# Optimization experiments

Hardware: AMD Instinct MI355X
Metric: run time of the kernel (lower is better)

## Reference

```python
import jax, jax.numpy as jnp
import numpy as np

B, VGEN, VINP, S, VOUT = 2048, 50000, 32000, 200, 50304


def setup_inputs() -> dict:
    key = jax.random.key(0)
    ks = jax.random.split(key, 7)
    gen_scores = jax.random.normal(ks[0], (B, VGEN), dtype=jnp.float32)   # unnormalized gen scores
    scores = jax.random.normal(ks[1], (B, S), dtype=jnp.float32)          # attention scores over input
    interp = jax.random.uniform(ks[2], (B, 1), dtype=jnp.float32)         # P(generate) vs P(copy)
    gen_zero_mask = jnp.ones((VGEN,), dtype=jnp.float32)                  # gen_zero mask (all-ones here)
    gen_to_out = jax.random.randint(ks[4], (VGEN,), 0, VOUT)              # gen vocab -> out vocab map
    inp_to_out = jax.random.randint(ks[5], (VINP,), 0, VOUT)              # inp vocab -> out vocab map
    ctx_inp = jax.random.randint(ks[6], (B, S), 0, VINP)                  # source token ids
    return {
        "gen_scores": gen_scores,
        "scores": scores,
        "interp": interp,
        "gen_zero_mask": gen_zero_mask,
        "gen_to_out": gen_to_out,
        "inp_to_out": inp_to_out,
        "ctx_inp": ctx_inp,
    }


def reference(gen_scores, scores, interp, gen_zero_mask, gen_to_out, inp_to_out, ctx_inp):
    b = gen_scores.shape[0]
    # generation distribution over gen vocab, masked, scattered into output vocab
    gen_probs = jax.nn.softmax(gen_scores, axis=-1) * gen_zero_mask[None, :]   # (B, VGEN)
    out_gen = jnp.zeros((b, VOUT), dtype=gen_scores.dtype).at[:, gen_to_out].add(gen_probs)
    # pointer/copy distribution over source positions, scattered via token-id map
    alphas = jax.nn.softmax(scores, axis=-1)                                   # (B, S)
    ctx_out = inp_to_out[ctx_inp]                                              # (B, S) out-vocab ids
    rows = jnp.arange(b)[:, None]                                              # (B, 1)
    out_ptr = jnp.zeros((b, VOUT), dtype=scores.dtype).at[rows, ctx_out].add(alphas)
    # mixture of generate and copy distributions over shared output vocab
    return interp * out_gen + (1.0 - interp) * out_ptr
```

## Files before the change

kernel.cpp:

```cpp
#include <hip/hip_runtime.h>
#include <hip/hip_fp16.h>

constexpr int Bn    = 2048;
constexpr int VGEN  = 50000;
constexpr int S     = 200;
constexpr int VOUT  = 50304;
constexpr int BLK   = 1024;

constexpr size_t WS_COUNTS = 0;
constexpr size_t WS_OFF    = WS_COUNTS + sizeof(int) * VOUT;
constexpr size_t WS_CURSOR = WS_OFF + sizeof(int) * (VOUT + 1);
constexpr size_t WS_CSR    = WS_CURSOR + sizeof(int) * VOUT;

constexpr int EX_BYTES  = VGEN * 2;
constexpr int RED_OFF   = EX_BYTES;
constexpr int ALPHA_OFF = RED_OFF + 32 * 4;
constexpr int COUT_OFF  = ALPHA_OFF + S * 4;
constexpr int SMEM_SZ   = COUT_OFF + S * 4;


__global__ void hist_k(const int* __restrict__ g2o, int* __restrict__ counts) {
    int i = blockIdx.x * blockDim.x + threadIdx.x;
    if (i < VGEN) atomicAdd(&counts[g2o[i]], 1);
}

__global__ void scan_k(const int* __restrict__ counts, int* __restrict__ off,
                       int* __restrict__ cursor) {
    __shared__ int wsum[16];
    const int tid  = threadIdx.x;
    const int lane = tid & 63;
    const int wid  = tid >> 6;
    int carry = 0;
    for (int base = 0; base < VOUT; base += BLK) {
        int i = base + tid;
        int x = (i < VOUT) ? counts[i] : 0;
        int incl = x;
#pragma unroll
        for (int d = 1; d < 64; d <<= 1) {
            int t = __shfl_up(incl, d, 64);
            if (lane >= d) incl += t;
        }
        if (lane == 63) wsum[wid] = incl;
        __syncthreads();
        int woff = 0, tot = 0;
#pragma unroll
        for (int w = 0; w < 16; ++w) {
            int s = wsum[w];
            if (w < wid) woff += s;
            tot += s;
        }
        int excl = carry + woff + incl - x;
        if (i < VOUT) { off[i] = excl; cursor[i] = excl; }
        carry += tot;
        __syncthreads();
    }
    if (tid == 0) off[VOUT] = carry;
}

__global__ void fill_k(const int* __restrict__ g2o, int* __restrict__ cursor,
                       int* __restrict__ csr) {
    int i = blockIdx.x * blockDim.x + threadIdx.x;
    if (i < VGEN) {
        int v = g2o[i];
        int pos = atomicAdd(&cursor[v], 1);
        csr[pos] = i;
    }
}


__device__ __forceinline__ float block_reduce_sum(float v, float* red) {
    __syncthreads();
    const int lane = threadIdx.x & 63;
    const int wid  = threadIdx.x >> 6;
#pragma unroll
    for (int d = 32; d > 0; d >>= 1) v += __shfl_down(v, d, 64);
    if (lane == 0) red[wid] = v;
    __syncthreads();
    if (wid == 0) {
        float t = (lane < 16) ? red[lane] : 0.f;
#pragma unroll
        for (int d = 8; d > 0; d >>= 1) t += __shfl_down(t, d, 64);
        if (lane == 0) red[0] = t;
    }
    __syncthreads();
    return red[0];
}

__global__ __launch_bounds__(BLK) void pg_main(
    const float* __restrict__ gen_scores,
    const float* __restrict__ scores,
    const float* __restrict__ interp,
    const float* __restrict__ mask,
    const int* __restrict__ inp_to_out,
    const int* __restrict__ ctx_inp,
    const int* __restrict__ off,
    const int* __restrict__ csr,
    float* __restrict__ out)
{
    extern __shared__ char smem[];
    __half* ex    = (__half*)smem;
    float*  red   = (float*)(smem + RED_OFF);
    float*  alpha = (float*)(smem + ALPHA_OFF);
    int*    tgt   = (int*)(smem + COUT_OFF);

    const int tid = threadIdx.x;
    const int b   = blockIdx.x;
    const float* grow = gen_scores + (size_t)b * VGEN;

    float lsum = 0.f;
    const float4* g4 = (const float4*)grow;
    const float4* m4 = (const float4*)mask;
    for (int i = tid; i < VGEN / 4; i += BLK) {
        float4 x = g4[i];
        float4 m = m4[i];
        float e0 = __expf(x.x), e1 = __expf(x.y);
        float e2 = __expf(x.z), e3 = __expf(x.w);
        lsum += (e0 + e1) + (e2 + e3);
        __half2* h = (__half2*)(ex + i * 4);
        h[0] = __floats2half2_rn(e0 * m.x, e1 * m.y);
        h[1] = __floats2half2_rn(e2 * m.z, e3 * m.w);
    }
    const float gsum = block_reduce_sum(lsum, red);

    float e = 0.f;
    if (tid < S) e = __expf(scores[(size_t)b * S + tid]);
    const float ssum = block_reduce_sum(e, red);
    const float it = interp[b];
    if (tid < S) {
        alpha[tid] = (1.f - it) * e / ssum;
        tgt[tid]   = inp_to_out[ctx_inp[(size_t)b * S + tid]];
    }
    __syncthreads();

    const float inv = it / gsum;
    float* orow = out + (size_t)b * VOUT;
    for (int v = tid; v < VOUT; v += BLK) {
        int s0 = off[v];
        int s1 = off[v + 1];
        float acc = 0.f;
        for (int j = s0; j < s1; ++j) {
            acc += __half2float(ex[csr[j]]);
        }
        orow[v] = acc * inv;
    }
    __syncthreads();

    if (tid < S) atomicAdd(&orow[tgt[tid]], alpha[tid]);
}


extern "C" void kernel_launch(void* const* d_in, const int* in_sizes, int n_in,
                              void* d_out, int out_size, void* d_ws, size_t ws_size,
                              hipStream_t stream) {
    const float* gen_scores = (const float*)d_in[0];
    const float* scores     = (const float*)d_in[1];
    const float* interp     = (const float*)d_in[2];
    const float* mask       = (const float*)d_in[3];
    const int*   gen_to_out = (const int*)d_in[4];
    const int*   inp_to_out = (const int*)d_in[5];
    const int*   ctx_inp    = (const int*)d_in[6];
    float* out = (float*)d_out;

    char* ws = (char*)d_ws;
    int* counts = (int*)(ws + WS_COUNTS);
    int* off    = (int*)(ws + WS_OFF);
    int* cursor = (int*)(ws + WS_CURSOR);
    int* csr    = (int*)(ws + WS_CSR);

    hipMemsetAsync(counts, 0, sizeof(int) * VOUT, stream);
    hist_k<<<(VGEN + 255) / 256, 256, 0, stream>>>(gen_to_out, counts);
    scan_k<<<1, BLK, 0, stream>>>(counts, off, cursor);
    fill_k<<<(VGEN + 255) / 256, 256, 0, stream>>>(gen_to_out, cursor, csr);

    hipFuncSetAttribute((const void*)pg_main,
                        hipFuncAttributeMaxDynamicSharedMemorySize, SMEM_SZ);
    pg_main<<<Bn, BLK, SMEM_SZ, stream>>>(gen_scores, scores, interp, mask,
                                          inp_to_out, ctx_inp, off, csr, out);
}
```

Measured before the change: 1.090 ms.

## Scatter exponentials into CSR order in LDS so the gather reads contiguously

Instead of storing a CSR list of source indices and gathering ex[csr[j]] per output slot, the fill kernel now records each gen index's rank (ushort) inside its output bucket. The main kernel scatters each half-precision exponential directly to its ranked LDS position, so the output loop sums contiguous LDS entries with no csr global loads. The output loop also preloads four offset pairs per thread before accumulating. This swaps global index traffic for scattered 2-byte LDS writes, which may cause bank conflicts, and relies on VGEN fitting in 16 bits.

After: 888.4 us. 18.5% less time.

```diff
diff --git a/kernel.cpp b/kernel.cpp
--- a/kernel.cpp
+++ b/kernel.cpp
@@ -10,7 +10,8 @@
 constexpr size_t WS_COUNTS = 0;
 constexpr size_t WS_OFF    = WS_COUNTS + sizeof(int) * VOUT;
 constexpr size_t WS_CURSOR = WS_OFF + sizeof(int) * (VOUT + 1);
-constexpr size_t WS_CSR    = WS_CURSOR + sizeof(int) * VOUT;
+constexpr size_t WS_RANK_RAW = WS_CURSOR + sizeof(int) * VOUT;
+constexpr size_t WS_RANK   = (WS_RANK_RAW + 7) & ~size_t(7);
 
 constexpr int EX_BYTES  = VGEN * 2;
 constexpr int RED_OFF   = EX_BYTES;
@@ -58,12 +59,12 @@
 }
 
 __global__ void fill_k(const int* __restrict__ g2o, int* __restrict__ cursor,
-                       int* __restrict__ csr) {
+                       unsigned short* __restrict__ rank) {
     int i = blockIdx.x * blockDim.x + threadIdx.x;
     if (i < VGEN) {
         int v = g2o[i];
         int pos = atomicAdd(&cursor[v], 1);
-        csr[pos] = i;
+        rank[i] = (unsigned short)pos;
     }
 }
 
@@ -94,7 +95,7 @@
     const int* __restrict__ inp_to_out,
     const int* __restrict__ ctx_inp,
     const int* __restrict__ off,
-    const int* __restrict__ csr,
+    const unsigned short* __restrict__ rank,
     float* __restrict__ out)
 {
     extern __shared__ char smem[];
@@ -108,17 +109,20 @@
     const float* grow = gen_scores + (size_t)b * VGEN;
 
     float lsum = 0.f;
-    const float4* g4 = (const float4*)grow;
-    const float4* m4 = (const float4*)mask;
+    const float4*  g4 = (const float4*)grow;
+    const float4*  m4 = (const float4*)mask;
+    const ushort4* r4 = (const ushort4*)rank;
     for (int i = tid; i < VGEN / 4; i += BLK) {
-        float4 x = g4[i];
-        float4 m = m4[i];
+        float4  x = g4[i];
+        float4  m = m4[i];
+        ushort4 r = r4[i];
         float e0 = __expf(x.x), e1 = __expf(x.y);
         float e2 = __expf(x.z), e3 = __expf(x.w);
         lsum += (e0 + e1) + (e2 + e3);
-        __half2* h = (__half2*)(ex + i * 4);
-        h[0] = __floats2half2_rn(e0 * m.x, e1 * m.y);
-        h[1] = __floats2half2_rn(e2 * m.z, e3 * m.w);
+        ex[r.x] = __float2half_rn(e0 * m.x);
+        ex[r.y] = __float2half_rn(e1 * m.y);
+        ex[r.z] = __float2half_rn(e2 * m.z);
+        ex[r.w] = __float2half_rn(e3 * m.w);
     }
     const float gsum = block_reduce_sum(lsum, red);
 
@@ -134,14 +138,21 @@
 
     const float inv = it / gsum;
     float* orow = out + (size_t)b * VOUT;
-    for (int v = tid; v < VOUT; v += BLK) {
-        int s0 = off[v];
-        int s1 = off[v + 1];
-        float acc = 0.f;
-        for (int j = s0; j < s1; ++j) {
-            acc += __half2float(ex[csr[j]]);
+    for (int vbase = tid; vbase < VOUT; vbase += 4 * BLK) {
+        int s0[4], s1[4];
+#pragma unroll
+        for (int u = 0; u < 4; ++u) {
+            int v = vbase + u * BLK;
+            if (v < VOUT) { s0[u] = off[v]; s1[u] = off[v + 1]; }
+            else          { s0[u] = 0;      s1[u] = 0; }
         }
-        orow[v] = acc * inv;
+#pragma unroll
+        for (int u = 0; u < 4; ++u) {
+            int v = vbase + u * BLK;
+            float acc = 0.f;
+            for (int j = s0[u]; j < s1[u]; ++j) acc += __half2float(ex[j]);
+            if (v < VOUT) orow[v] = acc * inv;
+        }
     }
     __syncthreads();
 
@@ -165,15 +176,15 @@
     int* counts = (int*)(ws + WS_COUNTS);
     int* off    = (int*)(ws + WS_OFF);
     int* cursor = (int*)(ws + WS_CURSOR);
-    int* csr    = (int*)(ws + WS_CSR);
+    unsigned short* rank = (unsigned short*)(ws + WS_RANK);
 
     hipMemsetAsync(counts, 0, sizeof(int) * VOUT, stream);
     hist_k<<<(VGEN + 255) / 256, 256, 0, stream>>>(gen_to_out, counts);
     scan_k<<<1, BLK, 0, stream>>>(counts, off, cursor);
-    fill_k<<<(VGEN + 255) / 256, 256, 0, stream>>>(gen_to_out, cursor, csr);
+    fill_k<<<(VGEN + 255) / 256, 256, 0, stream>>>(gen_to_out, cursor, rank);
 
     hipFuncSetAttribute((const void*)pg_main,
                         hipFuncAttributeMaxDynamicSharedMemorySize, SMEM_SZ);
     pg_main<<<Bn, BLK, SMEM_SZ, stream>>>(gen_scores, scores, interp, mask,
-                                          inp_to_out, ctx_inp, off, csr, out);
+                                          inp_to_out, ctx_inp, off, rank, out);
 }
```
